# Performance work log

Measured on AMD Instinct MI355X. Metric: run time of the kernel, lower is better.

The kernel has to match this reference:

```python
import jax, jax.numpy as jnp
import numpy as np

BS, SEQ, HID = 16, 4096, 768
NUM_MENTIONS = 128
ENT_DIM = 256
ENT_VOCAB = 50000


def setup_inputs() -> dict:
    key = jax.random.key(0)
    k1, k2, k3, k4, k5, k6, k7 = jax.random.split(key, 7)
    sequence_output = jax.random.normal(k1, (BS, SEQ, HID), dtype=jnp.float32)
    # start/end span indices into the zero-padded cumsum (valid range [0, SEQ])
    raw = jax.random.randint(k2, (BS, NUM_MENTIONS, 2), 0, SEQ, dtype=jnp.int64)
    mention_spans = jnp.sort(raw, axis=-1)
    # labels[:, 0] = entity index, labels[:, 1] = status (>=0 => positive target)
    labels = jax.random.randint(k3, (BS, 2, NUM_MENTIONS), 0, ENT_VOCAB, dtype=jnp.int64)
    linear_w = 0.02 * jax.random.normal(k4, (ENT_DIM, HID), dtype=jnp.float32)
    linear_b = jnp.zeros((ENT_DIM,), dtype=jnp.float32)
    ent_emb_table = jax.random.normal(k5, (ENT_VOCAB, ENT_DIM), dtype=jnp.float32)
    return {
        "sequence_output": sequence_output,
        "linear_w": linear_w,
        "linear_b": linear_b,
        "ent_emb_table": ent_emb_table,
        "mention_spans": mention_spans,
        "labels": labels,
    }


def _mean_mention_vectors(seq, spans):
    # cumsum trick: span sum = padded_cumsum[end] - padded_cumsum[start]
    cs = jnp.cumsum(seq, axis=1)                                   # [B,S,H]
    padded = jnp.concatenate([jnp.zeros_like(cs[:, :1]), cs], 1)   # [B,S+1,H]
    b_idx = jnp.arange(seq.shape[0])[:, None, None]
    gathered = padded[b_idx, spans]                                # [B,M,2,H]
    sums = gathered[:, :, 1] - gathered[:, :, 0]                   # [B,M,H]
    lengths = (spans[:, :, 1] - spans[:, :, 0]).astype(seq.dtype)[..., None]
    return jnp.nan_to_num(sums / lengths)                          # zero-length spans -> 0


def reference(sequence_output, linear_w, linear_b, ent_emb_table, mention_spans, labels):
    mention_vectors = _mean_mention_vectors(sequence_output, mention_spans)  # [B,M,H]
    entity_vectors = jnp.einsum('bmh,eh->bme', mention_vectors, linear_w) + linear_b  # [B,M,E]

    entity_labels = labels[:, 0].reshape(-1)                       # [N]
    entity_status = labels[:, 1].reshape(-1)                       # [N]
    label_embs = ent_emb_table[entity_labels]                      # [N,E]
    ev = entity_vectors.reshape(-1, entity_vectors.shape[-1])      # [N,E]
    logits = ev @ label_embs.T                                     # [N,N]

    n = logits.shape[0]
    valid = (entity_status >= 0).astype(logits.dtype)              # ignore negatives
    logp = jax.nn.log_softmax(logits, axis=-1)
    per_row = -logp[jnp.arange(n), jnp.arange(n)]                  # in-batch contrastive targets
    loss = jnp.nan_to_num(jnp.sum(per_row * valid) / jnp.sum(valid))
    return loss, entity_vectors
```

## Files before the change

### kernel.cpp

```cpp
#include <hip/hip_runtime.h>
#include <hip/hip_bf16.h>
#include <math.h>
#include <float.h>

#define BSZ 16
#define SEQ 4096
#define HID 768
#define H4  192
#define NM  128
#define NSPAN 256
#define ENT 256
#define NTOT 2048
#define SC  64
#define NCH 64

typedef __attribute__((ext_vector_type(8))) short bfx8;
typedef __attribute__((ext_vector_type(4))) float f32x4;

static __device__ __forceinline__ unsigned short f2bf(float x) {
  unsigned int u = __float_as_uint(x);
  unsigned int r = (u + 0x7fff + ((u >> 16) & 1)) >> 16;
  return (unsigned short)r;
}

__global__ __launch_bounds__(192) void k1_scan_prep_kernel(
    const float* __restrict__ seq, const int* __restrict__ spans,
    float* __restrict__ W, float* __restrict__ P,
    const float* __restrict__ lw, unsigned short* __restrict__ LWb,
    const float* __restrict__ table, const int* __restrict__ labels,
    unsigned short* __restrict__ LEb) {
  int bid = blockIdx.x, t = threadIdx.x;

  if (bid >= BSZ * NCH) {
    int pb = bid - BSZ * NCH;
    for (int idx = pb * 192 + t; idx < ENT * HID; idx += 128 * 192)
      LWb[idx] = f2bf(lw[idx]);
    for (int idx = pb * 192 + t; idx < NTOT * 256; idx += 128 * 192) {
      int j = idx >> 8, e = idx & 255;
      int lab = labels[(j >> 7) * 256 + (j & 127)];
      LEb[idx] = f2bf(table[(size_t)lab * ENT + e]);
    }
    return;
  }

  int b = bid >> 6;
  int c = bid & 63;

  __shared__ int head[SC + 1];
  __shared__ int nxt[NSPAN];
  __shared__ unsigned int maskw[2];
  __shared__ int has_end;
  for (int i = t; i < SC + 1; i += 192) head[i] = -1;
  if (t < 2) maskw[t] = 0u;
  if (t == 0) has_end = 0;
  __syncthreads();
  for (int j = t; j < NSPAN; j += 192) {
    int e = spans[b * NSPAN + j];
    int ch = e >> 6; if (ch > NCH - 1) ch = NCH - 1;
    if (ch == c) {
      int off = e - c * SC;
      nxt[j] = atomicExch(&head[off], j);
      if (off < SC) atomicOr(&maskw[off >> 5], 1u << (off & 31));
      else has_end = 1;
    }
  }
  __syncthreads();
  unsigned long long mask = ((unsigned long long)maskw[1] << 32) | maskw[0];
  int emit_end = has_end;

  const float4* seq4 =
      reinterpret_cast<const float4*>(seq) + (size_t)(b * SEQ + c * SC) * H4 + t;
  float4* W4 = reinterpret_cast<float4*>(W);
  float4 acc = make_float4(0.f, 0.f, 0.f, 0.f);
#pragma unroll 8
  for (int s = 0; s < SC; ++s) {
    if (mask & (1ull << s)) {
      for (int p = head[s]; p != -1; p = nxt[p]) {
        W4[(size_t)(b * NSPAN + p) * H4 + t] = acc;
      }
    }
    float4 v = seq4[(size_t)s * H4];
    acc.x += v.x; acc.y += v.y; acc.z += v.z; acc.w += v.w;
  }
  if (emit_end) {
    for (int p = head[SC]; p != -1; p = nxt[p]) {
      W4[(size_t)(b * NSPAN + p) * H4 + t] = acc;
    }
  }
  reinterpret_cast<float4*>(P)[(size_t)(b * NCH + c) * H4 + t] = acc;
}

__global__ __launch_bounds__(192) void chunk_prefix_kernel(float* __restrict__ P) {
  int b = blockIdx.x;
  int h = threadIdx.x;
  float4* P4 = reinterpret_cast<float4*>(P) + (size_t)b * NCH * H4 + h;
  float4 run = make_float4(0.f, 0.f, 0.f, 0.f);
  for (int cb = 0; cb < NCH; cb += 16) {
    float4 v[16];
#pragma unroll
    for (int i = 0; i < 16; ++i) v[i] = P4[(size_t)(cb + i) * H4];
#pragma unroll
    for (int i = 0; i < 16; ++i) {
      P4[(size_t)(cb + i) * H4] = run;
      run.x += v[i].x; run.y += v[i].y; run.z += v[i].z; run.w += v[i].w;
    }
  }
}

#define APAD 776
__global__ __launch_bounds__(256) void ev_mfma_kernel(
    const float* __restrict__ W, const float* __restrict__ P,
    const int* __restrict__ spans, const unsigned short* __restrict__ LWb,
    const float* __restrict__ bias, unsigned short* __restrict__ EVb,
    float* __restrict__ out) {
  int t = threadIdx.x;
  int chalf = blockIdx.x & 1;
  int i0 = (blockIdx.x >> 1) * 16;

  __shared__ unsigned short Ab[16][APAD];

  const float4* W4 = reinterpret_cast<const float4*>(W);
  const float4* P4 = reinterpret_cast<const float4*>(P);
  for (int it = 0; it < 12; ++it) {
    int q = it * 256 + t;
    int r = q / H4, h = q - r * H4;
    int bm = i0 + r;
    int b = bm >> 7, m = bm & (NM - 1);
    int e0 = spans[bm * 2], e1 = spans[bm * 2 + 1];
    int c0 = e0 >> 6; if (c0 > NCH - 1) c0 = NCH - 1;
    int c1 = e1 >> 6; if (c1 > NCH - 1) c1 = NCH - 1;
    float4 p0 = P4[(size_t)(b * NCH + c0) * H4 + h];
    float4 p1 = P4[(size_t)(b * NCH + c1) * H4 + h];
    float4 w0 = W4[(size_t)(b * NSPAN + 2 * m) * H4 + h];
    float4 w1 = W4[(size_t)(b * NSPAN + 2 * m + 1) * H4 + h];
    int len = e1 - e0;
    float inv = len > 0 ? 1.f / (float)len : 0.f;
    ushort4 pk;
    pk.x = f2bf(((p1.x + w1.x) - (p0.x + w0.x)) * inv);
    pk.y = f2bf(((p1.y + w1.y) - (p0.y + w0.y)) * inv);
    pk.z = f2bf(((p1.z + w1.z) - (p0.z + w0.z)) * inv);
    pk.w = f2bf(((p1.w + w1.w) - (p0.w + w0.w)) * inv);
    *reinterpret_cast<ushort4*>(&Ab[r][h * 4]) = pk;
  }
  __syncthreads();

  int w = t >> 6, l = t & 63;
  int lr = l & 15, lg = l >> 4;

  f32x4 acc[2];
  acc[0] = (f32x4)(0.f); acc[1] = (f32x4)(0.f);

  for (int ks = 0; ks < 24; ++ks) {
    bfx8 a = *reinterpret_cast<const bfx8*>(&Ab[lr][ks * 32 + lg * 8]);
#pragma unroll
    for (int nt = 0; nt < 2; ++nt) {
      int col = chalf * 128 + w * 32 + nt * 16 + lr;
      bfx8 bf = *reinterpret_cast<const bfx8*>(
          &LWb[(size_t)col * HID + ks * 32 + lg * 8]);
      acc[nt] = __builtin_amdgcn_mfma_f32_16x16x32_bf16(a, bf, acc[nt], 0, 0, 0);
    }
  }

#pragma unroll
  for (int nt = 0; nt < 2; ++nt) {
    int col = chalf * 128 + w * 32 + nt * 16 + lr;
    float bv = bias[col];
#pragma unroll
    for (int r = 0; r < 4; ++r) {
      int row = i0 + lg * 4 + r;
      float v = acc[nt][r] + bv;
      out[1 + (size_t)row * ENT + col] = v;
      EVb[(size_t)row * ENT + col] = f2bf(v);
    }
  }
}

__global__ __launch_bounds__(256) void loss_mfma_kernel(
    const unsigned short* __restrict__ EVb, const unsigned short* __restrict__ LEb,
    float* __restrict__ Pmax, float* __restrict__ Psum,
    float* __restrict__ Pdiag) {
  int t = threadIdx.x;
  int bid = blockIdx.x;
  int ctile = bid & 3, rtile = bid >> 2;
  int i0 = rtile * 32, c0 = ctile * 512;

  __shared__ unsigned short Ab[32][264];
  __shared__ float redm[4][32], reds[4][32];

  for (int q = t; q < 1024; q += 256) {
    int r = q >> 5, c8 = q & 31;
    *reinterpret_cast<bfx8*>(&Ab[r][c8 * 8]) =
        *reinterpret_cast<const bfx8*>(&EVb[(size_t)(i0 + r) * ENT + c8 * 8]);
  }
  __syncthreads();

  int w = t >> 6, l = t & 63;
  int lr = l & 15, lg = l >> 4;

  f32x4 acc[2][8];
#pragma unroll
  for (int mt = 0; mt < 2; ++mt)
#pragma unroll
    for (int nt = 0; nt < 8; ++nt) acc[mt][nt] = (f32x4)(0.f);

  for (int ks = 0; ks < 8; ++ks) {
    bfx8 a0 = *reinterpret_cast<const bfx8*>(&Ab[lr][ks * 32 + lg * 8]);
    bfx8 a1 = *reinterpret_cast<const bfx8*>(&Ab[16 + lr][ks * 32 + lg * 8]);
#pragma unroll
    for (int nt = 0; nt < 8; ++nt) {
      int col = c0 + (w * 8 + nt) * 16 + lr;
      bfx8 bf = *reinterpret_cast<const bfx8*>(
          &LEb[(size_t)col * ENT + ks * 32 + lg * 8]);
      acc[0][nt] = __builtin_amdgcn_mfma_f32_16x16x32_bf16(a0, bf, acc[0][nt], 0, 0, 0);
      acc[1][nt] = __builtin_amdgcn_mfma_f32_16x16x32_bf16(a1, bf, acc[1][nt], 0, 0, 0);
    }
  }

#pragma unroll
  for (int mt = 0; mt < 2; ++mt) {
    float mrow[4], srow[4];
#pragma unroll
    for (int r = 0; r < 4; ++r) {
      float m = acc[mt][0][r];
#pragma unroll
      for (int nt = 1; nt < 8; ++nt) m = fmaxf(m, acc[mt][nt][r]);
      m = fmaxf(m, __shfl_xor(m, 1));
      m = fmaxf(m, __shfl_xor(m, 2));
      m = fmaxf(m, __shfl_xor(m, 4));
      m = fmaxf(m, __shfl_xor(m, 8));
      mrow[r] = m;
      float s = 0.f;
#pragma unroll
      for (int nt = 0; nt < 8; ++nt) s += expf(acc[mt][nt][r] - m);
      s += __shfl_xor(s, 1);
      s += __shfl_xor(s, 2);
      s += __shfl_xor(s, 4);
      s += __shfl_xor(s, 8);
      srow[r] = s;
    }
    if (lr == 0) {
#pragma unroll
      for (int r = 0; r < 4; ++r) {
        redm[w][mt * 16 + lg * 4 + r] = mrow[r];
        reds[w][mt * 16 + lg * 4 + r] = srow[r];
      }
    }
#pragma unroll
    for (int nt = 0; nt < 8; ++nt) {
#pragma unroll
      for (int r = 0; r < 4; ++r) {
        int grow = i0 + mt * 16 + lg * 4 + r;
        int gcol = c0 + (w * 8 + nt) * 16 + lr;
        if (gcol == grow) Pdiag[grow] = acc[mt][nt][r];
      }
    }
  }
  __syncthreads();
  if (t < 32) {
    int i = i0 + t;
    float M = redm[0][t];
    M = fmaxf(M, redm[1][t]); M = fmaxf(M, redm[2][t]); M = fmaxf(M, redm[3][t]);
    float S = reds[0][t] * expf(redm[0][t] - M) + reds[1][t] * expf(redm[1][t] - M) +
              reds[2][t] * expf(redm[2][t] - M) + reds[3][t] * expf(redm[3][t] - M);
    Pmax[(i << 2) | ctile] = M;
    Psum[(i << 2) | ctile] = S;
  }
}

__global__ __launch_bounds__(1024) void finalize_kernel(
    const float* __restrict__ Pmax, const float* __restrict__ Psum,
    const float* __restrict__ Pdiag, const int* __restrict__ labels,
    float* __restrict__ out) {
  int t = threadIdx.x;
  float ls = 0.f, cnt = 0.f;
  for (int i = t; i < NTOT; i += 1024) {
    float4 mx = reinterpret_cast<const float4*>(Pmax)[i];
    float4 sm = reinterpret_cast<const float4*>(Psum)[i];
    float M = fmaxf(fmaxf(mx.x, mx.y), fmaxf(mx.z, mx.w));
    float S = sm.x * expf(mx.x - M) + sm.y * expf(mx.y - M) +
              sm.z * expf(mx.z - M) + sm.w * expf(mx.w - M);
    float pr = (logf(S) + M) - Pdiag[i];
    int status = labels[(i >> 7) * 256 + 128 + (i & 127)];
    if (status >= 0) { ls += pr; cnt += 1.f; }
  }
  __shared__ float rs[1024], rc[1024];
  rs[t] = ls; rc[t] = cnt;
  __syncthreads();
  for (int o = 512; o > 0; o >>= 1) {
    if (t < o) { rs[t] += rs[t + o]; rc[t] += rc[t + o]; }
    __syncthreads();
  }
  if (t == 0) {
    float L = rc[0] > 0.f ? rs[0] / rc[0] : 0.f;
    if (isnan(L)) L = 0.f;
    if (isinf(L)) L = L > 0.f ? FLT_MAX : -FLT_MAX;
    out[0] = L;
  }
}

extern "C" void kernel_launch(void* const* d_in, const int* in_sizes, int n_in,
                              void* d_out, int out_size, void* d_ws,
                              size_t ws_size, hipStream_t stream) {
  const float* seq   = (const float*)d_in[0];
  const float* lw    = (const float*)d_in[1];
  const float* lb    = (const float*)d_in[2];
  const float* table = (const float*)d_in[3];
  const int* spans   = (const int*)d_in[4];
  const int* labels  = (const int*)d_in[5];
  float* out = (float*)d_out;
  float* ws = (float*)d_ws;

  float* W  = ws;
  float* P  = W + (size_t)BSZ * NSPAN * HID;
  float* Pmax = P + (size_t)BSZ * NCH * HID;
  float* Psum = Pmax + NTOT * 4;
  float* Pdiag = Psum + NTOT * 4;
  unsigned short* LWb = (unsigned short*)(Pdiag + NTOT);
  unsigned short* LEb = LWb + (size_t)ENT * HID;
  unsigned short* EVb = LEb + (size_t)NTOT * ENT;

  k1_scan_prep_kernel<<<BSZ * NCH + 128, 192, 0, stream>>>(
      seq, spans, W, P, lw, LWb, table, labels, LEb);
  chunk_prefix_kernel<<<BSZ, 192, 0, stream>>>(P);
  ev_mfma_kernel<<<256, 256, 0, stream>>>(W, P, spans, LWb, lb, EVb, out);
  loss_mfma_kernel<<<256, 256, 0, stream>>>(EVb, LEb, Pmax, Psum, Pdiag);
  finalize_kernel<<<1, 1024, 0, stream>>>(Pmax, Psum, Pdiag, labels, out);
}
```

Measured before the change: 82.23 us.

## Fuse entity-vector projection into loss kernel and vectorize bf16 prep

Merges the mention-to-entity projection kernel into the contrastive-loss kernel. Each block recomputes its 32-row entity-vector tile in shared memory instead of writing and re-reading a bf16 buffer, which removes one launch and the global round-trip. In exchange, each projection tile is recomputed four times (once per column tile), with more global reads of W/P and the weights, and the block uses more shared memory. The weight and embedding bf16 conversion in the prep kernel now loads float4 pairs and writes 8-wide packed stores instead of scalar ones.

```diff
diff --git a/kernel.cpp b/kernel.cpp
--- a/kernel.cpp
+++ b/kernel.cpp
@@ -23,6 +23,15 @@
   return (unsigned short)r;
 }
 
+static __device__ __forceinline__ bfx8 pack8(float4 v0, float4 v1) {
+  bfx8 p;
+  p[0] = (short)f2bf(v0.x); p[1] = (short)f2bf(v0.y);
+  p[2] = (short)f2bf(v0.z); p[3] = (short)f2bf(v0.w);
+  p[4] = (short)f2bf(v1.x); p[5] = (short)f2bf(v1.y);
+  p[6] = (short)f2bf(v1.z); p[7] = (short)f2bf(v1.w);
+  return p;
+}
+
 __global__ __launch_bounds__(192) void k1_scan_prep_kernel(
     const float* __restrict__ seq, const int* __restrict__ spans,
     float* __restrict__ W, float* __restrict__ P,
@@ -32,13 +41,19 @@
   int bid = blockIdx.x, t = threadIdx.x;
 
   if (bid >= BSZ * NCH) {
-    int pb = bid - BSZ * NCH;
-    for (int idx = pb * 192 + t; idx < ENT * HID; idx += 128 * 192)
-      LWb[idx] = f2bf(lw[idx]);
-    for (int idx = pb * 192 + t; idx < NTOT * 256; idx += 128 * 192) {
-      int j = idx >> 8, e = idx & 255;
+    int tid = (bid - BSZ * NCH) * 192 + t;
+    {
+      const float4* s = reinterpret_cast<const float4*>(lw) + (size_t)tid * 2;
+      float4 v0 = s[0], v1 = s[1];
+      *reinterpret_cast<bfx8*>(LWb + (size_t)tid * 8) = pack8(v0, v1);
+    }
+    for (int i8 = tid; i8 < NTOT * 32; i8 += 24576) {
+      int j = i8 >> 5, e8 = i8 & 31;
       int lab = labels[(j >> 7) * 256 + (j & 127)];
-      LEb[idx] = f2bf(table[(size_t)lab * ENT + e]);
+      const float4* s =
+          reinterpret_cast<const float4*>(table + (size_t)lab * ENT) + e8 * 2;
+      float4 v0 = s[0], v1 = s[1];
+      *reinterpret_cast<bfx8*>(LEb + (size_t)j * ENT + e8 * 8) = pack8(v0, v1);
     }
     return;
   }
@@ -108,29 +123,33 @@
 }
 
 #define APAD 776
-__global__ __launch_bounds__(256) void ev_mfma_kernel(
+__global__ __launch_bounds__(256) void fused_ev_loss_kernel(
     const float* __restrict__ W, const float* __restrict__ P,
     const int* __restrict__ spans, const unsigned short* __restrict__ LWb,
-    const float* __restrict__ bias, unsigned short* __restrict__ EVb,
-    float* __restrict__ out) {
+    const float* __restrict__ bias, const unsigned short* __restrict__ LEb,
+    float* __restrict__ Pmax, float* __restrict__ Psum,
+    float* __restrict__ Pdiag, float* __restrict__ out) {
   int t = threadIdx.x;
-  int chalf = blockIdx.x & 1;
-  int i0 = (blockIdx.x >> 1) * 16;
-
-  __shared__ unsigned short Ab[16][APAD];
+  int bid = blockIdx.x;
+  int ctile = bid & 3, rtile = bid >> 2;
+  int i0 = rtile * 32, c0 = ctile * 512;
+
+  __shared__ unsigned short Ab[32][APAD];
+  __shared__ unsigned short A2[32][264];
+  __shared__ float redm[4][32], reds[4][32];
 
   const float4* W4 = reinterpret_cast<const float4*>(W);
   const float4* P4 = reinterpret_cast<const float4*>(P);
-  for (int it = 0; it < 12; ++it) {
+  for (int it = 0; it < 24; ++it) {
     int q = it * 256 + t;
     int r = q / H4, h = q - r * H4;
     int bm = i0 + r;
     int b = bm >> 7, m = bm & (NM - 1);
     int e0 = spans[bm * 2], e1 = spans[bm * 2 + 1];
-    int c0 = e0 >> 6; if (c0 > NCH - 1) c0 = NCH - 1;
-    int c1 = e1 >> 6; if (c1 > NCH - 1) c1 = NCH - 1;
-    float4 p0 = P4[(size_t)(b * NCH + c0) * H4 + h];
-    float4 p1 = P4[(size_t)(b * NCH + c1) * H4 + h];
+    int cc0 = e0 >> 6; if (cc0 > NCH - 1) cc0 = NCH - 1;
+    int cc1 = e1 >> 6; if (cc1 > NCH - 1) cc1 = NCH - 1;
+    float4 p0 = P4[(size_t)(b * NCH + cc0) * H4 + h];
+    float4 p1 = P4[(size_t)(b * NCH + cc1) * H4 + h];
     float4 w0 = W4[(size_t)(b * NSPAN + 2 * m) * H4 + h];
     float4 w1 = W4[(size_t)(b * NSPAN + 2 * m + 1) * H4 + h];
     int len = e1 - e0;
@@ -147,55 +166,41 @@
   int w = t >> 6, l = t & 63;
   int lr = l & 15, lg = l >> 4;
 
-  f32x4 acc[2];
-  acc[0] = (f32x4)(0.f); acc[1] = (f32x4)(0.f);
-
-  for (int ks = 0; ks < 24; ++ks) {
-    bfx8 a = *reinterpret_cast<const bfx8*>(&Ab[lr][ks * 32 + lg * 8]);
-#pragma unroll
-    for (int nt = 0; nt < 2; ++nt) {
-      int col = chalf * 128 + w * 32 + nt * 16 + lr;
-      bfx8 bf = *reinterpret_cast<const bfx8*>(
-          &LWb[(size_t)col * HID + ks * 32 + lg * 8]);
-      acc[nt] = __builtin_amdgcn_mfma_f32_16x16x32_bf16(a, bf, acc[nt], 0, 0, 0);
-    }
-  }
-
-#pragma unroll
-  for (int nt = 0; nt < 2; ++nt) {
-    int col = chalf * 128 + w * 32 + nt * 16 + lr;
-    float bv = bias[col];
-#pragma unroll
-    for (int r = 0; r < 4; ++r) {
-      int row = i0 + lg * 4 + r;
-      float v = acc[nt][r] + bv;
-      out[1 + (size_t)row * ENT + col] = v;
-      EVb[(size_t)row * ENT + col] = f2bf(v);
-    }
-  }
-}
-
-__global__ __launch_bounds__(256) void loss_mfma_kernel(
-    const unsigned short* __restrict__ EVb, const unsigned short* __restrict__ LEb,
-    float* __restrict__ Pmax, float* __restrict__ Psum,
-    float* __restrict__ Pdiag) {
-  int t = threadIdx.x;
-  int bid = blockIdx.x;
-  int ctile = bid & 3, rtile = bid >> 2;
-  int i0 = rtile * 32, c0 = ctile * 512;
-
-  __shared__ unsigned short Ab[32][264];
-  __shared__ float redm[4][32], reds[4][32];
-
-  for (int q = t; q < 1024; q += 256) {
-    int r = q >> 5, c8 = q & 31;
-    *reinterpret_cast<bfx8*>(&Ab[r][c8 * 8]) =
-        *reinterpret_cast<const bfx8*>(&EVb[(size_t)(i0 + r) * ENT + c8 * 8]);
-  }
-  __syncthreads();
-
-  int w = t >> 6, l = t & 63;
-  int lr = l & 15, lg = l >> 4;
+  {
+    f32x4 eacc[2][4];
+#pragma unroll
+    for (int mt = 0; mt < 2; ++mt)
+#pragma unroll
+      for (int nt = 0; nt < 4; ++nt) eacc[mt][nt] = (f32x4)(0.f);
+    for (int ks = 0; ks < 24; ++ks) {
+      bfx8 a0 = *reinterpret_cast<const bfx8*>(&Ab[lr][ks * 32 + lg * 8]);
+      bfx8 a1 = *reinterpret_cast<const bfx8*>(&Ab[16 + lr][ks * 32 + lg * 8]);
+#pragma unroll
+      for (int nt = 0; nt < 4; ++nt) {
+        int col = w * 64 + nt * 16 + lr;
+        bfx8 bf = *reinterpret_cast<const bfx8*>(
+            &LWb[(size_t)col * HID + ks * 32 + lg * 8]);
+        eacc[0][nt] = __builtin_amdgcn_mfma_f32_16x16x32_bf16(a0, bf, eacc[0][nt], 0, 0, 0);
+        eacc[1][nt] = __builtin_amdgcn_mfma_f32_16x16x32_bf16(a1, bf, eacc[1][nt], 0, 0, 0);
+      }
+    }
+#pragma unroll
+    for (int mt = 0; mt < 2; ++mt) {
+#pragma unroll
+      for (int nt = 0; nt < 4; ++nt) {
+        int col = w * 64 + nt * 16 + lr;
+        float bv = bias[col];
+#pragma unroll
+        for (int r = 0; r < 4; ++r) {
+          int row = mt * 16 + lg * 4 + r;
+          float v = eacc[mt][nt][r] + bv;
+          A2[row][col] = f2bf(v);
+          if (ctile == 0) out[1 + (size_t)(i0 + row) * ENT + col] = v;
+        }
+      }
+    }
+  }
+  __syncthreads();
 
   f32x4 acc[2][8];
 #pragma unroll
@@ -204,8 +209,8 @@
     for (int nt = 0; nt < 8; ++nt) acc[mt][nt] = (f32x4)(0.f);
 
   for (int ks = 0; ks < 8; ++ks) {
-    bfx8 a0 = *reinterpret_cast<const bfx8*>(&Ab[lr][ks * 32 + lg * 8]);
-    bfx8 a1 = *reinterpret_cast<const bfx8*>(&Ab[16 + lr][ks * 32 + lg * 8]);
+    bfx8 a0 = *reinterpret_cast<const bfx8*>(&A2[lr][ks * 32 + lg * 8]);
+    bfx8 a1 = *reinterpret_cast<const bfx8*>(&A2[16 + lr][ks * 32 + lg * 8]);
 #pragma unroll
     for (int nt = 0; nt < 8; ++nt) {
       int col = c0 + (w * 8 + nt) * 16 + lr;
@@ -317,12 +322,11 @@
   float* Pdiag = Psum + NTOT * 4;
   unsigned short* LWb = (unsigned short*)(Pdiag + NTOT);
   unsigned short* LEb = LWb + (size_t)ENT * HID;
-  unsigned short* EVb = LEb + (size_t)NTOT * ENT;
 
   k1_scan_prep_kernel<<<BSZ * NCH + 128, 192, 0, stream>>>(
       seq, spans, W, P, lw, LWb, table, labels, LEb);
   chunk_prefix_kernel<<<BSZ, 192, 0, stream>>>(P);
-  ev_mfma_kernel<<<256, 256, 0, stream>>>(W, P, spans, LWb, lb, EVb, out);
-  loss_mfma_kernel<<<256, 256, 0, stream>>>(EVb, LEb, Pmax, Psum, Pdiag);
+  fused_ev_loss_kernel<<<256, 256, 0, stream>>>(
+      W, P, spans, LWb, lb, LEb, Pmax, Psum, Pdiag, out);
   finalize_kernel<<<1, 1024, 0, stream>>>(Pmax, Psum, Pdiag, labels, out);
 }
```

After: 95.32 us. +15.9%, slower.
